# Performance work log

Measured on AMD Instinct MI355X. Metric: run time of the kernel, lower is better.

Reference implementation:

```python
import jax, jax.numpy as jnp
import numpy as np

EMBED = 1024
HEADS = 16
HEAD_DIM = EMBED // HEADS
HIDDEN = 4 * EMBED
EPS = 1e-5


def setup_inputs() -> dict:
    key = jax.random.key(0)
    ks = jax.random.split(key, 9)
    s = lambda fan_in: 1.0 / np.sqrt(fan_in)
    inp = {
        "x": jax.random.normal(ks[0], (2, 2048, EMBED), dtype=jnp.float32),
        "ln1_w": jnp.ones((EMBED,), jnp.float32),
        "ln1_b": jnp.zeros((EMBED,), jnp.float32),
        "ln2_w": jnp.ones((EMBED,), jnp.float32),
        "ln2_b": jnp.zeros((EMBED,), jnp.float32),
        "qkv_w": jax.random.uniform(ks[1], (EMBED, 3 * EMBED), jnp.float32, -s(EMBED), s(EMBED)),
        "qkv_b": jax.random.uniform(ks[2], (3 * EMBED,), jnp.float32, -s(EMBED), s(EMBED)),
        "proj_w": jax.random.uniform(ks[3], (EMBED, EMBED), jnp.float32, -s(EMBED), s(EMBED)),
        "proj_b": jax.random.uniform(ks[4], (EMBED,), jnp.float32, -s(EMBED), s(EMBED)),
        "fc1_w": jax.random.uniform(ks[5], (EMBED, HIDDEN), jnp.float32, -s(EMBED), s(EMBED)),
        "fc1_b": jax.random.uniform(ks[6], (HIDDEN,), jnp.float32, -s(EMBED), s(EMBED)),
        "fc2_w": jax.random.uniform(ks[7], (HIDDEN, EMBED), jnp.float32, -s(HIDDEN), s(HIDDEN)),
        "fc2_b": jax.random.uniform(ks[8], (EMBED,), jnp.float32, -s(HIDDEN), s(HIDDEN)),
    }
    return inp


def _layernorm(x, w, b):
    mu = jnp.mean(x, axis=-1, keepdims=True)
    var = jnp.mean(jnp.square(x - mu), axis=-1, keepdims=True)
    return (x - mu) * jax.lax.rsqrt(var + EPS) * w + b


def _attn(x, qkv_w, qkv_b, proj_w, proj_b):
    B, N, C = x.shape
    qkv = x @ qkv_w + qkv_b                      # [B,N,3C]
    qkv = qkv.reshape(B, N, 3, HEADS, HEAD_DIM)
    q, k, v = qkv[:, :, 0], qkv[:, :, 1], qkv[:, :, 2]   # [B,N,H,D]
    scale = HEAD_DIM ** -0.5
    scores = jnp.einsum("bqhd,bkhd->bhqk", q, k) * scale  # [B,H,N,N]
    attn = jax.nn.softmax(scores, axis=-1)
    out = jnp.einsum("bhqk,bkhd->bqhd", attn, v).reshape(B, N, C)
    return out @ proj_w + proj_b


def _mlp(x, fc1_w, fc1_b, fc2_w, fc2_b):
    h = jax.nn.gelu(x @ fc1_w + fc1_b, approximate=False)
    return h @ fc2_w + fc2_b


def reference(x, ln1_w, ln1_b, ln2_w, ln2_b, qkv_w, qkv_b, proj_w, proj_b,
              fc1_w, fc1_b, fc2_w, fc2_b):
    # pre-norm transformer block (eval mode: dropout/drop_path are identity)
    x = x + _attn(_layernorm(x, ln1_w, ln1_b), qkv_w, qkv_b, proj_w, proj_b)
    x = x + _mlp(_layernorm(x, ln2_w, ln2_b), fc1_w, fc1_b, fc2_w, fc2_b)
    return x
```

## Files before the change

### kernel.cpp

```cpp
#include <hip/hip_runtime.h>
#include <hip/hip_bf16.h>

#define SEQ    2048
#define BATCH  2
#define MTOK   4096
#define EMBED  1024
#define HEADS  16
#define HDIM   64
#define QKV3   3072
#define FFN    4096

typedef __attribute__((ext_vector_type(8))) short bf16x8;
typedef __attribute__((ext_vector_type(4))) float f32x4;

static __device__ __forceinline__ unsigned short f2bf(float f) {
  union { float f; unsigned u; } x; x.f = f;
  unsigned r = x.u + 0x7FFFu + ((x.u >> 16) & 1u);
  return (unsigned short)(r >> 16);
}
static __device__ __forceinline__ float bf2f(unsigned short u) {
  union { unsigned u; float f; } x; x.u = ((unsigned)u) << 16; return x.f;
}
static __device__ __forceinline__ unsigned pk2bf(float a, float b) {
#if __has_builtin(__builtin_amdgcn_cvt_pk_bf16_f32)
  typedef __attribute__((ext_vector_type(2))) __bf16 bf16x2_t;
  union { bf16x2_t v; unsigned u; } x;
  x.v = __builtin_amdgcn_cvt_pk_bf16_f32(a, b);
  return x.u;
#else
  return ((unsigned)f2bf(a)) | (((unsigned)f2bf(b)) << 16);
#endif
}

static __device__ __forceinline__ void gload16(const unsigned short* g, unsigned short* l) {
  __builtin_amdgcn_global_load_lds((const __attribute__((address_space(1))) void*)g,
                                   (__attribute__((address_space(3))) void*)l, 16, 0, 0);
}

struct TD { const float* W; unsigned short* T; int K, N, ntx, base; };
struct TD4 { TD d[4]; };

__global__ void transpose_all(TD4 td) {
  __shared__ float t[32][33];
  int bid = blockIdx.x;
  int i = 0;
  if (bid >= td.d[1].base) i = 1;
  if (bid >= td.d[2].base) i = 2;
  if (bid >= td.d[3].base) i = 3;
  const TD& D = td.d[i];
  int local = bid - D.base;
  int n0 = (local % D.ntx) * 32, k0 = (local / D.ntx) * 32;
  int tx = threadIdx.x, ty = threadIdx.y;
#pragma unroll
  for (int j = 0; j < 32; j += 8)
    t[ty + j][tx] = D.W[(size_t)(k0 + ty + j) * D.N + n0 + tx];
  __syncthreads();
#pragma unroll
  for (int j = 0; j < 32; j += 8)
    D.T[(size_t)(n0 + ty + j) * D.K + k0 + tx] = f2bf(t[tx][ty + j]);
}

__global__ __launch_bounds__(256) void ln_kernel(const float* __restrict__ in,
                                                 const float* __restrict__ w,
                                                 const float* __restrict__ b,
                                                 unsigned short* __restrict__ out) {
  __shared__ float sh[4];
  int row = blockIdx.x, tid = threadIdx.x;
  const float4 v = ((const float4*)(in + (size_t)row * EMBED))[tid];
  float s = v.x + v.y + v.z + v.w;
#pragma unroll
  for (int off = 32; off; off >>= 1) s += __shfl_xor(s, off);
  if ((tid & 63) == 0) sh[tid >> 6] = s;
  __syncthreads();
  float mean = (sh[0] + sh[1] + sh[2] + sh[3]) * (1.0f / EMBED);
  __syncthreads();
  float dx = v.x - mean, dy = v.y - mean, dz = v.z - mean, dw = v.w - mean;
  float q = dx * dx + dy * dy + dz * dz + dw * dw;
#pragma unroll
  for (int off = 32; off; off >>= 1) q += __shfl_xor(q, off);
  if ((tid & 63) == 0) sh[tid >> 6] = q;
  __syncthreads();
  float var = (sh[0] + sh[1] + sh[2] + sh[3]) * (1.0f / EMBED);
  float rs = rsqrtf(var + 1e-5f);
  const float4 wv = ((const float4*)w)[tid];
  const float4 bv = ((const float4*)b)[tid];
  ushort4 o;
  o.x = f2bf(dx * rs * wv.x + bv.x);
  o.y = f2bf(dy * rs * wv.y + bv.y);
  o.z = f2bf(dz * rs * wv.z + bv.z);
  o.w = f2bf(dw * rs * wv.w + bv.w);
  ((ushort4*)(out + (size_t)row * EMBED))[tid] = o;
}

template <int ACT, int OUTBF, int VSPLIT>
__global__ __launch_bounds__(256) void gemmBig(const unsigned short* __restrict__ A,
                                               const unsigned short* __restrict__ Wt,
                                               const float* __restrict__ bias,
                                               unsigned short* __restrict__ outB,
                                               float* __restrict__ outF,
                                               unsigned short* __restrict__ vT,
                                               int M, int N, int K, int nblk) {
  __shared__ __align__(16) unsigned short As[128 * 64];
  __shared__ __align__(16) unsigned short Bs[128 * 64];
  const int tid = threadIdx.x;
  const int wave = tid >> 6, lane = tid & 63;
  const int quad = lane >> 4, ml = lane & 15;
  const int wr = wave >> 1, wc = wave & 1;
  const int m0 = (blockIdx.x / nblk) * 128;
  const int n0 = (blockIdx.x % nblk) * 128;
  const int srow = lane >> 3;
  const int schunk = (lane & 7) ^ (srow & 7);
  const unsigned short* Ag = A + (size_t)(m0 + wave * 32 + srow) * K + schunk * 8;
  const unsigned short* Bg = Wt + (size_t)(n0 + wave * 32 + srow) * K + schunk * 8;
  unsigned short* AsW = &As[wave * 2048];
  unsigned short* BsW = &Bs[wave * 2048];
  f32x4 acc[4][4];
#pragma unroll
  for (int i = 0; i < 4; i++)
#pragma unroll
    for (int j = 0; j < 4; j++) acc[i][j] = (f32x4){0.f, 0.f, 0.f, 0.f};
  for (int k0 = 0; k0 < K; k0 += 64) {
    __syncthreads();
#pragma unroll
    for (int t = 0; t < 4; t++) {
      gload16(Ag + (size_t)(8 * t) * K, AsW + 512 * t);
      gload16(Bg + (size_t)(8 * t) * K, BsW + 512 * t);
    }
    Ag += 64; Bg += 64;
    __syncthreads();
#pragma unroll
    for (int kh = 0; kh < 2; kh++) {
      const int ch = ((kh * 4 + quad) ^ (ml & 7)) * 8;
      bf16x8 af[4], bfr[4];
#pragma unroll
      for (int mt = 0; mt < 4; mt++)
        af[mt] = *(const bf16x8*)&As[(wr * 64 + mt * 16 + ml) * 64 + ch];
#pragma unroll
      for (int nt = 0; nt < 4; nt++)
        bfr[nt] = *(const bf16x8*)&Bs[(wc * 64 + nt * 16 + ml) * 64 + ch];
#pragma unroll
      for (int mt = 0; mt < 4; mt++)
#pragma unroll
        for (int nt = 0; nt < 4; nt++)
          acc[mt][nt] = __builtin_amdgcn_mfma_f32_16x16x32_bf16(af[mt], bfr[nt], acc[mt][nt], 0, 0, 0);
    }
  }
#pragma unroll
  for (int mt = 0; mt < 4; mt++)
#pragma unroll
    for (int nt = 0; nt < 4; nt++) {
      const int col0 = n0 + wc * 64 + nt * 16;
      const int row0 = m0 + wr * 64 + mt * 16;
      if (VSPLIT && col0 >= 2 * EMBED) {
        const int b = row0 >> 11, tok0 = row0 & (SEQ - 1);
        const int h = (col0 - 2 * EMBED) >> 6;
        const int dl = ((col0 - 2 * EMBED) & 63) + ml;
        float bia = bias[col0 + ml];
        ushort4 o;
        o.x = f2bf(acc[mt][nt][0] + bia);
        o.y = f2bf(acc[mt][nt][1] + bia);
        o.z = f2bf(acc[mt][nt][2] + bia);
        o.w = f2bf(acc[mt][nt][3] + bia);
        *(ushort4*)(vT + (size_t)((b * 16 + h) * 64 + dl) * SEQ + tok0 + quad * 4) = o;
      } else {
#pragma unroll
        for (int r = 0; r < 4; r++) {
          int row = row0 + quad * 4 + r;
          int col = col0 + ml;
          float v = acc[mt][nt][r] + bias[col];
          if (ACT) v = 0.5f * v * (1.0f + erff(v * 0.70710678118f));
          if (OUTBF)
            outB[(size_t)row * N + col] = f2bf(v);
          else
            outF[(size_t)row * N + col] = v;
        }
      }
    }
}

template <int RES, int OUTBF>
__global__ __launch_bounds__(256) void gemm64k(const unsigned short* __restrict__ A,
                                               const unsigned short* __restrict__ Wt,
                                               const float* __restrict__ bias,
                                               const float* __restrict__ res,
                                               unsigned short* __restrict__ outB,
                                               float* __restrict__ outF,
                                               int M, int N, int K, int nblk) {
  __shared__ __align__(16) unsigned short As[128 * 64];
  __shared__ __align__(16) unsigned short Bs[64 * 64];
  const int tid = threadIdx.x;
  const int wave = tid >> 6, lane = tid & 63;
  const int quad = lane >> 4, ml = lane & 15;
  const int wr = wave >> 1, wc = wave & 1;
  const int xcd = blockIdx.x & 7, idx = blockIdx.x >> 3;
  const int mPerXcd = (gridDim.x >> 3) / nblk;
  const int m0 = (xcd * mPerXcd + idx / nblk) * 128;
  const int n0 = (idx % nblk) * 64;
  const int srow = lane >> 3;
  const int schunk = (lane & 7) ^ (srow & 7);
  const unsigned short* Ag = A + (size_t)(m0 + wave * 32 + srow) * K + schunk * 8;
  const unsigned short* Bg = Wt + (size_t)(n0 + wave * 16 + srow) * K + schunk * 8;
  unsigned short* AsW = &As[wave * 2048];
  unsigned short* BsW = &Bs[wave * 1024];
  f32x4 acc[4][2];
#pragma unroll
  for (int i = 0; i < 4; i++) { acc[i][0] = (f32x4){0.f,0.f,0.f,0.f}; acc[i][1] = acc[i][0]; }
  for (int k0 = 0; k0 < K; k0 += 64) {
    __syncthreads();
    gload16(Ag, AsW);
    gload16(Ag + (size_t)8 * K,  AsW + 512);
    gload16(Ag + (size_t)16 * K, AsW + 1024);
    gload16(Ag + (size_t)24 * K, AsW + 1536);
    gload16(Bg, BsW);
    gload16(Bg + (size_t)8 * K,  BsW + 512);
    Ag += 64; Bg += 64;
    __syncthreads();
#pragma unroll
    for (int kh = 0; kh < 2; kh++) {
      const int ch = ((kh * 4 + quad) ^ (ml & 7)) * 8;
      bf16x8 af[4], bfr[2];
#pragma unroll
      for (int mt = 0; mt < 4; mt++)
        af[mt] = *(const bf16x8*)&As[(wr * 64 + mt * 16 + ml) * 64 + ch];
#pragma unroll
      for (int nt = 0; nt < 2; nt++)
        bfr[nt] = *(const bf16x8*)&Bs[(wc * 32 + nt * 16 + ml) * 64 + ch];
#pragma unroll
      for (int mt = 0; mt < 4; mt++)
#pragma unroll
        for (int nt = 0; nt < 2; nt++)
          acc[mt][nt] = __builtin_amdgcn_mfma_f32_16x16x32_bf16(af[mt], bfr[nt], acc[mt][nt], 0, 0, 0);
    }
  }
#pragma unroll
  for (int mt = 0; mt < 4; mt++)
#pragma unroll
    for (int nt = 0; nt < 2; nt++)
#pragma unroll
      for (int r = 0; r < 4; r++) {
        int row = m0 + wr * 64 + mt * 16 + quad * 4 + r;
        int col = n0 + wc * 32 + nt * 16 + ml;
        float v = acc[mt][nt][r] + bias[col];
        if (RES) v += res[(size_t)row * N + col];
        if (OUTBF)
          outB[(size_t)row * N + col] = f2bf(v);
        else
          outF[(size_t)row * N + col] = v;
      }
}

#define PS 72
__global__ __launch_bounds__(256) void attn_kernel(const unsigned short* __restrict__ qkv,
                                                   const unsigned short* __restrict__ vT,
                                                   unsigned short* __restrict__ attn) {
  __shared__ __align__(16) unsigned short Ks[64 * 64];
  __shared__ __align__(16) unsigned short Vs[64 * 64];
  __shared__ __align__(16) unsigned short Ps[4][16 * PS];
  const int tid = threadIdx.x, wave = tid >> 6, lane = tid & 63;
  const int quad = lane >> 4, ml = lane & 15;
  const int bh = blockIdx.x, b = bh >> 4, h = bh & 15;
  const int q0 = blockIdx.y * 64 + wave * 16;
  const float qscale = 0.18033688011112042f;
  const unsigned short* qrow = qkv + (size_t)(b * SEQ + q0 + ml) * QKV3 + h * HDIM;
  bf16x8 aq0 = *(const bf16x8*)(qrow + quad * 8);
  bf16x8 aq1 = *(const bf16x8*)(qrow + 32 + quad * 8);
#pragma unroll
  for (int j = 0; j < 8; j++) {
    aq0[j] = (short)f2bf(bf2f((unsigned short)aq0[j]) * qscale);
    aq1[j] = (short)f2bf(bf2f((unsigned short)aq1[j]) * qscale);
  }
  bf16x8 ones;
#pragma unroll
  for (int j = 0; j < 8; j++) ones[j] = (short)0x3F80;
  f32x4 O[4], lsum = {0.f, 0.f, 0.f, 0.f};
#pragma unroll
  for (int i = 0; i < 4; i++) O[i] = (f32x4){0.f, 0.f, 0.f, 0.f};
  const int skey = lane >> 3;
  const int schunk8 = (((lane & 7) ^ ((lane >> 3) & 7))) * 8;
  const int swz = (ml & 7);
  const unsigned short* kbase =
      qkv + (size_t)(b * SEQ + wave * 16 + skey) * QKV3 + EMBED + h * HDIM + schunk8;
  const unsigned short* vbase =
      vT + (size_t)(bh * 64 + wave * 16 + skey) * SEQ + schunk8;
  unsigned short* KsW = &Ks[wave * 1024];
  unsigned short* VsW = &Vs[wave * 1024];
  for (int kt = 0; kt < SEQ; kt += 64) {
    __syncthreads();
    gload16(kbase + (size_t)kt * QKV3, KsW);
    gload16(kbase + (size_t)(kt + 8) * QKV3, KsW + 512);
    gload16(vbase + kt, VsW);
    gload16(vbase + kt + (size_t)8 * SEQ, VsW + 512);
    __syncthreads();
#pragma unroll
    for (int s = 0; s < 4; s++) {
      bf16x8 blo = *(const bf16x8*)&Ks[(s * 16 + ml) * 64 + (quad ^ swz) * 8];
      bf16x8 bhi = *(const bf16x8*)&Ks[(s * 16 + ml) * 64 + ((4 + quad) ^ swz) * 8];
      f32x4 St = {0.f, 0.f, 0.f, 0.f};
      St = __builtin_amdgcn_mfma_f32_16x16x32_bf16(blo, aq0, St, 0, 0, 0);
      St = __builtin_amdgcn_mfma_f32_16x16x32_bf16(bhi, aq1, St, 0, 0, 0);
      uint2 pk_;
      pk_.x = pk2bf(exp2f(St[0]), exp2f(St[1]));
      pk_.y = pk2bf(exp2f(St[2]), exp2f(St[3]));
      *(uint2*)&Ps[wave][ml * PS + s * 16 + quad * 4] = pk_;
    }
    bf16x8 ap0 = *(const bf16x8*)&Ps[wave][ml * PS + quad * 8];
    bf16x8 ap1 = *(const bf16x8*)&Ps[wave][ml * PS + 32 + quad * 8];
    lsum = __builtin_amdgcn_mfma_f32_16x16x32_bf16(ap0, ones, lsum, 0, 0, 0);
    lsum = __builtin_amdgcn_mfma_f32_16x16x32_bf16(ap1, ones, lsum, 0, 0, 0);
#pragma unroll
    for (int d = 0; d < 4; d++) {
      bf16x8 bv0 = *(const bf16x8*)&Vs[(d * 16 + ml) * 64 + (quad ^ swz) * 8];
      bf16x8 bv1 = *(const bf16x8*)&Vs[(d * 16 + ml) * 64 + ((4 + quad) ^ swz) * 8];
      O[d] = __builtin_amdgcn_mfma_f32_16x16x32_bf16(ap0, bv0, O[d], 0, 0, 0);
      O[d] = __builtin_amdgcn_mfma_f32_16x16x32_bf16(ap1, bv1, O[d], 0, 0, 0);
    }
  }
#pragma unroll
  for (int r = 0; r < 4; r++) {
    float inv = 1.0f / lsum[r];
    size_t g = (size_t)(b * SEQ + q0 + quad * 4 + r) * EMBED + h * HDIM + ml;
    attn[g + 0]  = f2bf(O[0][r] * inv);
    attn[g + 16] = f2bf(O[1][r] * inv);
    attn[g + 32] = f2bf(O[2][r] * inv);
    attn[g + 48] = f2bf(O[3][r] * inv);
  }
}

extern "C" void kernel_launch(void* const* d_in, const int* in_sizes, int n_in,
                              void* d_out, int out_size, void* d_ws, size_t ws_size,
                              hipStream_t stream) {
  const float* x      = (const float*)d_in[0];
  const float* ln1_w  = (const float*)d_in[1];
  const float* ln1_b  = (const float*)d_in[2];
  const float* ln2_w  = (const float*)d_in[3];
  const float* ln2_b  = (const float*)d_in[4];
  const float* qkv_w  = (const float*)d_in[5];
  const float* qkv_b  = (const float*)d_in[6];
  const float* proj_w = (const float*)d_in[7];
  const float* proj_b = (const float*)d_in[8];
  const float* fc1_w  = (const float*)d_in[9];
  const float* fc1_b  = (const float*)d_in[10];
  const float* fc2_w  = (const float*)d_in[11];
  const float* fc2_b  = (const float*)d_in[12];
  float* out = (float*)d_out;
  char* wsb = (char*)d_ws;
  unsigned short* lnbuf  = (unsigned short*)(wsb + 0);
  unsigned short* qkvb   = (unsigned short*)(wsb + 8388608);
  unsigned short* attnb  = (unsigned short*)(wsb + 33554432);
  unsigned short* vTb    = (unsigned short*)(wsb + 41943040);
  unsigned short* actb   = (unsigned short*)(wsb + 33554432);
  float*          h1     = (float*)(wsb + 67108864);
  unsigned short* qkvWt  = (unsigned short*)(wsb + 83886080);
  unsigned short* projWt = (unsigned short*)(wsb + 90177536);
  unsigned short* fc1Wt  = (unsigned short*)(wsb + 92274688);
  unsigned short* fc2Wt  = (unsigned short*)(wsb + 100663296);

  TD4 td;
  td.d[0] = {qkv_w,  qkvWt,  1024, 3072,  96, 0};
  td.d[1] = {proj_w, projWt, 1024, 1024,  32, 3072};
  td.d[2] = {fc1_w,  fc1Wt,  1024, 4096, 128, 4096};
  td.d[3] = {fc2_w,  fc2Wt,  4096, 1024,  32, 8192};
  transpose_all<<<12288, dim3(32, 8), 0, stream>>>(td);

  ln_kernel<<<MTOK, 256, 0, stream>>>(x, ln1_w, ln1_b, lnbuf);
  gemmBig<0, 1, 1><<<768, 256, 0, stream>>>(
      lnbuf, qkvWt, qkv_b, qkvb, nullptr, vTb, MTOK, QKV3, EMBED, 24);
  attn_kernel<<<dim3(32, 32), 256, 0, stream>>>(qkvb, vTb, attnb);
  gemm64k<1, 0><<<512, 256, 0, stream>>>(
      attnb, projWt, proj_b, x, nullptr, h1, MTOK, EMBED, EMBED, 16);
  ln_kernel<<<MTOK, 256, 0, stream>>>(h1, ln2_w, ln2_b, lnbuf);
  gemmBig<1, 1, 0><<<1024, 256, 0, stream>>>(
      lnbuf, fc1Wt, fc1_b, actb, nullptr, nullptr, MTOK, FFN, EMBED, 32);
  gemm64k<1, 0><<<512, 256, 0, stream>>>(
      actb, fc2Wt, fc2_b, h1, nullptr, out, MTOK, EMBED, FFN, 16);
}
```

Before: 383.1 us.

## Double-buffer K/V tiles in attention and swizzle P scratch layout

Attention now double-buffers the K and V shared-memory tiles, issuing the next tile's direct-to-LDS loads before computing on the current tile, and needs only one barrier per iteration. The P scratch buffer drops its padding and uses an XOR-swizzled layout instead. Exp2 switches to the hardware intrinsic, and wave priority is raised around the PV MFMAs. The intent is to hide global load latency behind compute, at the cost of twice the LDS for K/V, which may reduce occupancy.

```diff
diff --git a/kernel.cpp b/kernel.cpp
--- a/kernel.cpp
+++ b/kernel.cpp
@@ -29,6 +29,13 @@
   return x.u;
 #else
   return ((unsigned)f2bf(a)) | (((unsigned)f2bf(b)) << 16);
+#endif
+}
+static __device__ __forceinline__ float fexp2(float x) {
+#if __has_builtin(__builtin_amdgcn_exp2f)
+  return __builtin_amdgcn_exp2f(x);
+#else
+  return exp2f(x);
 #endif
 }
 
@@ -249,13 +256,12 @@
       }
 }
 
-#define PS 72
 __global__ __launch_bounds__(256) void attn_kernel(const unsigned short* __restrict__ qkv,
                                                    const unsigned short* __restrict__ vT,
                                                    unsigned short* __restrict__ attn) {
-  __shared__ __align__(16) unsigned short Ks[64 * 64];
-  __shared__ __align__(16) unsigned short Vs[64 * 64];
-  __shared__ __align__(16) unsigned short Ps[4][16 * PS];
+  __shared__ __align__(16) unsigned short Ks[2][64 * 64];
+  __shared__ __align__(16) unsigned short Vs[2][64 * 64];
+  __shared__ __align__(16) unsigned short Ps[4][16 * 64];
   const int tid = threadIdx.x, wave = tid >> 6, lane = tid & 63;
   const int quad = lane >> 4, ml = lane & 15;
   const int bh = blockIdx.x, b = bh >> 4, h = bh & 15;
@@ -282,38 +288,54 @@
       qkv + (size_t)(b * SEQ + wave * 16 + skey) * QKV3 + EMBED + h * HDIM + schunk8;
   const unsigned short* vbase =
       vT + (size_t)(bh * 64 + wave * 16 + skey) * SEQ + schunk8;
-  unsigned short* KsW = &Ks[wave * 1024];
-  unsigned short* VsW = &Vs[wave * 1024];
-  for (int kt = 0; kt < SEQ; kt += 64) {
-    __syncthreads();
-    gload16(kbase + (size_t)kt * QKV3, KsW);
-    gload16(kbase + (size_t)(kt + 8) * QKV3, KsW + 512);
-    gload16(vbase + kt, VsW);
-    gload16(vbase + kt + (size_t)8 * SEQ, VsW + 512);
-    __syncthreads();
+  unsigned short* PsW = &Ps[wave][0];
+
+  gload16(kbase, &Ks[0][wave * 1024]);
+  gload16(kbase + (size_t)8 * QKV3, &Ks[0][wave * 1024] + 512);
+  gload16(vbase, &Vs[0][wave * 1024]);
+  gload16(vbase + (size_t)8 * SEQ, &Vs[0][wave * 1024] + 512);
+  __syncthreads();
+
+  for (int kti = 0; kti < SEQ / 64; ++kti) {
+    const int cur = kti & 1;
+    if (kti + 1 < SEQ / 64) {
+      const int kt = (kti + 1) * 64;
+      unsigned short* kd = &Ks[cur ^ 1][wave * 1024];
+      unsigned short* vd = &Vs[cur ^ 1][wave * 1024];
+      gload16(kbase + (size_t)kt * QKV3, kd);
+      gload16(kbase + (size_t)(kt + 8) * QKV3, kd + 512);
+      gload16(vbase + kt, vd);
+      gload16(vbase + kt + (size_t)8 * SEQ, vd + 512);
+    }
+    const unsigned short* Kc = &Ks[cur][0];
+    const unsigned short* Vc = &Vs[cur][0];
 #pragma unroll
     for (int s = 0; s < 4; s++) {
-      bf16x8 blo = *(const bf16x8*)&Ks[(s * 16 + ml) * 64 + (quad ^ swz) * 8];
-      bf16x8 bhi = *(const bf16x8*)&Ks[(s * 16 + ml) * 64 + ((4 + quad) ^ swz) * 8];
+      bf16x8 blo = *(const bf16x8*)&Kc[(s * 16 + ml) * 64 + (quad ^ swz) * 8];
+      bf16x8 bhi = *(const bf16x8*)&Kc[(s * 16 + ml) * 64 + ((4 + quad) ^ swz) * 8];
       f32x4 St = {0.f, 0.f, 0.f, 0.f};
       St = __builtin_amdgcn_mfma_f32_16x16x32_bf16(blo, aq0, St, 0, 0, 0);
       St = __builtin_amdgcn_mfma_f32_16x16x32_bf16(bhi, aq1, St, 0, 0, 0);
       uint2 pk_;
-      pk_.x = pk2bf(exp2f(St[0]), exp2f(St[1]));
-      pk_.y = pk2bf(exp2f(St[2]), exp2f(St[3]));
-      *(uint2*)&Ps[wave][ml * PS + s * 16 + quad * 4] = pk_;
-    }
-    bf16x8 ap0 = *(const bf16x8*)&Ps[wave][ml * PS + quad * 8];
-    bf16x8 ap1 = *(const bf16x8*)&Ps[wave][ml * PS + 32 + quad * 8];
+      pk_.x = pk2bf(fexp2(St[0]), fexp2(St[1]));
+      pk_.y = pk2bf(fexp2(St[2]), fexp2(St[3]));
+      const int chs = (2 * s + (quad >> 1)) ^ swz;
+      *(uint2*)((char*)PsW + ml * 128 + chs * 16 + (quad & 1) * 8) = pk_;
+    }
+    bf16x8 ap0 = *(const bf16x8*)((const char*)PsW + ml * 128 + ((quad ^ swz) << 4));
+    bf16x8 ap1 = *(const bf16x8*)((const char*)PsW + ml * 128 + (((4 + quad) ^ swz) << 4));
+    __builtin_amdgcn_s_setprio(1);
     lsum = __builtin_amdgcn_mfma_f32_16x16x32_bf16(ap0, ones, lsum, 0, 0, 0);
     lsum = __builtin_amdgcn_mfma_f32_16x16x32_bf16(ap1, ones, lsum, 0, 0, 0);
 #pragma unroll
     for (int d = 0; d < 4; d++) {
-      bf16x8 bv0 = *(const bf16x8*)&Vs[(d * 16 + ml) * 64 + (quad ^ swz) * 8];
-      bf16x8 bv1 = *(const bf16x8*)&Vs[(d * 16 + ml) * 64 + ((4 + quad) ^ swz) * 8];
+      bf16x8 bv0 = *(const bf16x8*)&Vs[cur][(d * 16 + ml) * 64 + (quad ^ swz) * 8];
+      bf16x8 bv1 = *(const bf16x8*)&Vc[(d * 16 + ml) * 64 + ((4 + quad) ^ swz) * 8];
       O[d] = __builtin_amdgcn_mfma_f32_16x16x32_bf16(ap0, bv0, O[d], 0, 0, 0);
       O[d] = __builtin_amdgcn_mfma_f32_16x16x32_bf16(ap1, bv1, O[d], 0, 0, 0);
     }
+    __builtin_amdgcn_s_setprio(0);
+    __syncthreads();
   }
 #pragma unroll
   for (int r = 0; r < 4; r++) {
```

New measurement: 365.0 us. -4.7%, faster.
